# Optimization experiments

Measured on AMD Instinct MI355X. Metric: run time of the kernel, lower is better.

The kernel has to match this reference:

```python
import jax, jax.numpy as jnp
import numpy as np

N = 65536      # number of nodes being updated
EMBED = 1024   # embed_size
G = 256        # g_size (per-head dim)
MLP = 256      # mlp_size
H = 4          # n_head


def setup_inputs() -> dict:
    key = jax.random.key(0)
    ks = jax.random.split(key, 8)
    s_in = 1.0 / np.sqrt(EMBED)
    s_g = 1.0 / np.sqrt(G)
    s_m = 1.0 / np.sqrt(MLP)
    s_hg = 1.0 / np.sqrt(H * G)
    return {
        "q": jax.random.normal(ks[0], (N, EMBED), jnp.float32),
        "rep": jax.random.normal(ks[1], (N, EMBED), jnp.float32),
        "Wq": jax.random.normal(ks[2], (EMBED, H * G), jnp.float32) * s_in,
        "Wk": jax.random.normal(ks[3], (EMBED, H * G), jnp.float32) * s_in,
        "Wv": jax.random.normal(ks[4], (EMBED, H * G), jnp.float32) * s_in,
        "W1": jax.random.normal(ks[5], (H, G, MLP), jnp.float32) * s_g,
        "b1": jnp.zeros((H, MLP), jnp.float32),
        "W2": jax.random.normal(ks[6], (H, MLP, G), jnp.float32) * s_m,
        "b2": jnp.zeros((H, G), jnp.float32),
        "Ws": jax.random.normal(ks[7], (H * G, EMBED), jnp.float32) * s_hg,
    }


def reference(q, rep, Wq, Wk, Wv, W1, b1, W2, b2, Ws):
    # Per-head Q/K/V projections: [N, E] -> [N, H, G]
    n = q.shape[0]
    Qh = (q @ Wq).reshape(n, H, G)
    Kh = (rep @ Wk).reshape(n, H, G)
    Vh = (rep @ Wv).reshape(n, H, G)
    # Elementwise scaled attention gate (Q, K are per-node vectors -> 2D attn)
    gate = jax.nn.sigmoid(Qh * Kh * (1.0 / np.sqrt(G)))
    z = gate * Vh  # [N, H, G]
    # Per-head MLP (num_mlp = 1 block): G -> MLP -> G with ReLU
    h1 = jax.nn.relu(jnp.einsum('nhg,hgm->nhm', z, W1) + b1)
    z2 = jnp.einsum('nhm,hmg->nhg', h1, W2) + b2
    update_gate = z2.reshape(n, H * G)
    # update_attn_scale (no bias) + fused residual: h = Q - K + proj(gate)
    h = q - rep + update_gate @ Ws
    return h
```

## Files before the change

kernel.cpp:

```cpp
#include <hip/hip_runtime.h>
#include <hip/hip_bf16.h>


typedef __attribute__((ext_vector_type(8))) short bf16x8;
typedef __attribute__((ext_vector_type(4))) float f32x4;
typedef __attribute__((ext_vector_type(4))) short short4v;

static __device__ __forceinline__ short f2b(float x) {
  __hip_bfloat16 h = __float2bfloat16(x);
  return __builtin_bit_cast(short, h);
}
static __device__ __forceinline__ float b2f(short s) {
  unsigned u = ((unsigned)(unsigned short)s) << 16;
  return __builtin_bit_cast(float, u);
}

static __device__ __forceinline__ void stage_half(
    const short* __restrict__ g, long ld, short* dst, int wave, int lane)
{
  const int rw = lane >> 2;
  const int gg = (lane & 3) ^ ((rw >> 1) & 3);
  const short* gl = g + (long)rw * ld + (gg << 3);
  #pragma unroll
  for (int j = 0; j < 2; ++j) {
    const int r0 = j * 128 + wave * 16;
    __builtin_amdgcn_global_load_lds(
        (const __attribute__((address_space(1))) void*)(gl + (long)r0 * ld),
        (__attribute__((address_space(3))) void*)(dst + r0 * 32),
        16, 0, 0);
  }
}

static __device__ __forceinline__ void stage_half128(
    const short* __restrict__ g, long ld, short* dst, int wave, int lane)
{
  const int rw = lane >> 2;
  const int gg = (lane & 3) ^ ((rw >> 1) & 3);
  const int r0 = wave * 16;
  __builtin_amdgcn_global_load_lds(
      (const __attribute__((address_space(1))) void*)(g + (long)(r0 + rw) * ld + (gg << 3)),
      (__attribute__((address_space(3))) void*)(dst + r0 * 32),
      16, 0, 0);
}

__global__ void cvt_bf16(const float* __restrict__ in, short* __restrict__ out, long n) {
  long i = ((long)blockIdx.x * blockDim.x + threadIdx.x) * 4;
  const long stride = (long)gridDim.x * blockDim.x * 4;
  for (; i < n; i += stride) {
    float4 v = *(const float4*)(in + i);
    short4v o = { f2b(v.x), f2b(v.y), f2b(v.z), f2b(v.w) };
    *(short4v*)(out + i) = o;
  }
}

__global__ void prep_weights(
    const float* __restrict__ Wq, const float* __restrict__ Wk, const float* __restrict__ Wv,
    const float* __restrict__ W1, const float* __restrict__ W2, const float* __restrict__ Ws,
    short* __restrict__ wqt, short* __restrict__ wkt, short* __restrict__ wvt,
    short* __restrict__ w1t, short* __restrict__ w2t, short* __restrict__ wst)
{
  const int job = blockIdx.z;
  const float* src; short* dst; int R, C;
  if (job < 3)       { src = (job==0)?Wq:((job==1)?Wk:Wv); dst = (job==0)?wqt:((job==1)?wkt:wvt); R = 1024; C = 1024; }
  else if (job == 3) { src = Ws; dst = wst; R = 1024; C = 1024; }
  else if (job < 8)  { int h = job-4; src = W1 + h*65536; dst = w1t + h*65536; R = 256; C = 256; }
  else               { int h = job-8; src = W2 + h*65536; dst = w2t + h*65536; R = 256; C = 256; }
  const int c0 = blockIdx.x * 32, r0 = blockIdx.y * 32;
  if (c0 >= C || r0 >= R) return;
  __shared__ float t[32][33];
  for (int i = threadIdx.y; i < 32; i += 8)
    t[i][threadIdx.x] = src[(long)(r0 + i) * C + c0 + threadIdx.x];
  __syncthreads();
  for (int i = threadIdx.y; i < 32; i += 8)
    dst[(long)(c0 + i) * R + r0 + threadIdx.x] = f2b(t[threadIdx.x][i]);
}

template <int KDIM, bool RELU, bool BIAS, bool RESID, bool SWZ>
__global__ __launch_bounds__(512, 2) void gemm_bf16(
    const short* __restrict__ A, long lda, long zsa,
    const short* __restrict__ Bt, long ldb, long zsb,
    void* __restrict__ outv, long ldc, long zsc,
    const float* __restrict__ bias, long zsbias,
    const short* __restrict__ qres, const short* __restrict__ rres)
{
  __shared__ __align__(16) short lA[2][2][8192];
  __shared__ __align__(16) short lB[2][2][8192];
  const int lane = threadIdx.x & 63, wave = threadIdx.x >> 6;
  const int wm = wave >> 2, wn = wave & 3;
  int bx = blockIdx.x, by = blockIdx.y;
  if (SWZ) {
    const int nbx = gridDim.x;
    const int flat = by * nbx + bx;
    const int chunk = (int)(gridDim.x * gridDim.y) >> 3;
    const int fid = (flat & 7) * chunk + (flat >> 3);
    bx = fid % nbx; by = fid / nbx;
  }
  const long bm = (long)by * 256;
  const int  bn = bx * 256;
  const int  zi = blockIdx.z;

  const short* Ab = A + (long)zi * zsa + bm * lda;
  const short* Bb = Bt + (long)zi * zsb + (long)bn * ldb;
  constexpr int NT = KDIM / 64;
  const int g0 = lane >> 4;
  const int arow = wm * 128 + (lane & 15);
  const int bcol = wn * 64 + (lane & 15);

  auto stA = [&](int buf, int ks, int t) {
    const int tc = t < NT ? t : NT - 1;
    stage_half(Ab + tc * 64 + ks * 32, lda, &lA[buf][ks][0], wave, lane);
  };
  auto stB = [&](int buf, int ks, int t) {
    const int tc = t < NT ? t : NT - 1;
    stage_half(Bb + tc * 64 + ks * 32, ldb, &lB[buf][ks][0], wave, lane);
  };

  stA(0, 0, 0); stB(0, 0, 0); stA(0, 1, 0); stB(0, 1, 0);
  stA(1, 0, 1); stB(1, 0, 1);
  asm volatile("s_waitcnt vmcnt(4)" ::: "memory");
  __builtin_amdgcn_s_barrier();

  f32x4 acc[8][4] = {};
  bf16x8 b[4];

#define PHASE(BUF, MH, KS, LOADB, STAGE_STMT, CHECK)                        \
  {                                                                         \
    const short* aS = &lA[BUF][KS][0];                                      \
    const short* bS = &lB[BUF][KS][0];                                      \
    if (LOADB) {                                                            \
      _Pragma("unroll")                                                     \
      for (int j = 0; j < 4; ++j) {                                         \
        const int c = bcol + j * 16;                                        \
        b[j] = *(const bf16x8*)(bS + c * 32 + (((g0 ^ (c >> 1)) & 3) << 3));\
      }                                                                     \
    }                                                                       \
    bf16x8 a[4];                                                            \
    _Pragma("unroll")                                                       \
    for (int i2 = 0; i2 < 4; ++i2) {                                        \
      const int r = arow + (MH) * 64 + i2 * 16;                             \
      a[i2] = *(const bf16x8*)(aS + r * 32 + (((g0 ^ (r >> 1)) & 3) << 3)); \
    }                                                                       \
    STAGE_STMT;                                                             \
    if (CHECK) asm volatile("s_waitcnt vmcnt(4)" ::: "memory");             \
    asm volatile("" ::: "memory");                                          \
    __builtin_amdgcn_s_barrier();                                           \
    asm volatile("s_waitcnt lgkmcnt(0)" ::: "memory");                      \
    __builtin_amdgcn_sched_barrier(0);                                      \
    __builtin_amdgcn_s_setprio(1);                                          \
    _Pragma("unroll")                                                       \
    for (int i2 = 0; i2 < 4; ++i2)                                          \
      _Pragma("unroll")                                                     \
      for (int j = 0; j < 4; ++j)                                           \
        acc[(MH) * 4 + i2][j] = __builtin_amdgcn_mfma_f32_16x16x32_bf16(    \
            a[i2], b[j], acc[(MH) * 4 + i2][j], 0, 0, 0);                   \
    __builtin_amdgcn_s_setprio(0);                                          \
    asm volatile("" ::: "memory");                                          \
    __builtin_amdgcn_s_barrier();                                           \
  }

  for (int t = 0; t < NT; t += 2) {
    PHASE(0, 0, 0, true,  stA(1, 1, t + 1), false)
    PHASE(0, 1, 0, false, stB(1, 1, t + 1), false)
    PHASE(0, 0, 1, true,  stA(0, 0, t + 2), false)
    PHASE(0, 1, 1, false, stB(0, 0, t + 2), true)
    PHASE(1, 0, 0, true,  stA(0, 1, t + 2), false)
    PHASE(1, 1, 0, false, stB(0, 1, t + 2), false)
    PHASE(1, 0, 1, true,  stA(1, 0, t + 3), false)
    PHASE(1, 1, 1, false, stB(1, 0, t + 3), true)
  }
#undef PHASE

  #pragma unroll
  for (int i = 0; i < 8; ++i)
    #pragma unroll
    for (int j = 0; j < 4; ++j)
      #pragma unroll
      for (int r = 0; r < 4; ++r) {
        const int rl = wm * 128 + i * 16 + ((lane >> 4) << 2) + r;
        const int cl = wn * 64 + j * 16 + (lane & 15);
        float v = acc[i][j][r];
        if (BIAS) v += bias[(long)zi * zsbias + bn + cl];
        if (RELU) v = v > 0.0f ? v : 0.0f;
        const long row = bm + rl;
        const long gi = (long)zi * zsc + row * ldc + bn + cl;
        if (RESID) {
          ((float*)outv)[gi] = b2f(qres[gi]) - b2f(rres[gi]) + v;
        } else {
          ((short*)outv)[gi] = f2b(v);
        }
      }
}

__global__ __launch_bounds__(512, 2) void gemm_g23(
    const short* __restrict__ rb,
    const short* __restrict__ wkt,
    const short* __restrict__ wvt,
    const short* __restrict__ gh,
    short* __restrict__ zb)
{
  __shared__ __align__(16) short lA[2][2][8192];
  __shared__ __align__(16) short lK[2][2][4096];
  __shared__ __align__(16) short lV[2][2][4096];
  const int lane = threadIdx.x & 63, wave = threadIdx.x >> 6;
  const int wm = wave >> 2, wn = wave & 3;
  int bx = blockIdx.x, by = blockIdx.y;
  {
    const int flat = by * 8 + bx;
    const int chunk = (int)(gridDim.x * gridDim.y) >> 3;
    const int fid = (flat & 7) * chunk + (flat >> 3);
    bx = fid & 7; by = fid >> 3;
  }
  const long bm = (long)by * 256;
  const int  bn = bx * 128;

  const short* Ab = rb + bm * 1024;
  const short* Kb = wkt + (long)bn * 1024;
  const short* Vb = wvt + (long)bn * 1024;
  constexpr int NT = 16;
  const int g0 = lane >> 4;
  const int arow = wm * 128 + (lane & 15);
  const int bcol = wn * 32 + (lane & 15);

  auto stA = [&](int buf, int ks, int t) {
    const int tc = t < NT ? t : NT - 1;
    stage_half(Ab + tc * 64 + ks * 32, 1024, &lA[buf][ks][0], wave, lane);
  };
  auto stK = [&](int buf, int ks, int t) {
    const int tc = t < NT ? t : NT - 1;
    stage_half128(Kb + tc * 64 + ks * 32, 1024, &lK[buf][ks][0], wave, lane);
  };
  auto stV = [&](int buf, int ks, int t) {
    const int tc = t < NT ? t : NT - 1;
    stage_half128(Vb + tc * 64 + ks * 32, 1024, &lV[buf][ks][0], wave, lane);
  };

  stA(0, 0, 0); stK(0, 0, 0); stV(0, 0, 0);
  stA(0, 1, 0); stK(0, 1, 0); stV(0, 1, 0);
  stA(1, 0, 1); stK(1, 0, 1); stV(1, 0, 1);
  asm volatile("s_waitcnt vmcnt(4)" ::: "memory");
  __builtin_amdgcn_s_barrier();

  f32x4 ack[8][2] = {};
  f32x4 acv[8][2] = {};
  bf16x8 bk[2], bv[2];

#define PHASEG(BUF, MH, KS, LOADB, STAGE_STMT, CHECK)                       \
  {                                                                         \
    const short* aS = &lA[BUF][KS][0];                                      \
    if (LOADB) {                                                            \
      _Pragma("unroll")                                                     \
      for (int j = 0; j < 2; ++j) {                                         \
        const int c = bcol + j * 16;                                        \
        const int so = c * 32 + (((g0 ^ (c >> 1)) & 3) << 3);               \
        bk[j] = *(const bf16x8*)(&lK[BUF][KS][0] + so);                     \
        bv[j] = *(const bf16x8*)(&lV[BUF][KS][0] + so);                     \
      }                                                                     \
    }                                                                       \
    bf16x8 a[4];                                                            \
    _Pragma("unroll")                                                       \
    for (int i2 = 0; i2 < 4; ++i2) {                                        \
      const int r = arow + (MH) * 64 + i2 * 16;                             \
      a[i2] = *(const bf16x8*)(aS + r * 32 + (((g0 ^ (r >> 1)) & 3) << 3)); \
    }                                                                       \
    STAGE_STMT;                                                             \
    if (CHECK) asm volatile("s_waitcnt vmcnt(4)" ::: "memory");             \
    asm volatile("" ::: "memory");                                          \
    __builtin_amdgcn_s_barrier();                                           \
    asm volatile("s_waitcnt lgkmcnt(0)" ::: "memory");                      \
    __builtin_amdgcn_sched_barrier(0);                                      \
    __builtin_amdgcn_s_setprio(1);                                          \
    _Pragma("unroll")                                                       \
    for (int i2 = 0; i2 < 4; ++i2)                                          \
      _Pragma("unroll")                                                     \
      for (int j = 0; j < 2; ++j) {                                         \
        ack[(MH) * 4 + i2][j] = __builtin_amdgcn_mfma_f32_16x16x32_bf16(    \
            a[i2], bk[j], ack[(MH) * 4 + i2][j], 0, 0, 0);                  \
        acv[(MH) * 4 + i2][j] = __builtin_amdgcn_mfma_f32_16x16x32_bf16(    \
            a[i2], bv[j], acv[(MH) * 4 + i2][j], 0, 0, 0);                  \
      }                                                                     \
    __builtin_amdgcn_s_setprio(0);                                          \
    asm volatile("" ::: "memory");                                          \
    __builtin_amdgcn_s_barrier();                                           \
  }

  for (int t = 0; t < NT; t += 2) {
    PHASEG(0, 0, 0, true,  stA(1, 1, t + 1), false)
    PHASEG(0, 1, 0, false, { stK(1, 1, t + 1); stV(1, 1, t + 1); }, false)
    PHASEG(0, 0, 1, true,  stA(0, 0, t + 2), false)
    PHASEG(0, 1, 1, false, { stK(0, 0, t + 2); stV(0, 0, t + 2); }, true)
    PHASEG(1, 0, 0, true,  stA(0, 1, t + 2), false)
    PHASEG(1, 1, 0, false, { stK(0, 1, t + 2); stV(0, 1, t + 2); }, false)
    PHASEG(1, 0, 1, true,  stA(1, 0, t + 3), false)
    PHASEG(1, 1, 1, false, { stK(1, 0, t + 3); stV(1, 0, t + 3); }, true)
  }
#undef PHASEG

  #pragma unroll
  for (int i = 0; i < 8; ++i)
    #pragma unroll
    for (int j = 0; j < 2; ++j)
      #pragma unroll
      for (int r = 0; r < 4; ++r) {
        const int rl = wm * 128 + i * 16 + ((lane >> 4) << 2) + r;
        const int cl = wn * 32 + j * 16 + (lane & 15);
        const long gi = (bm + rl) * 1024 + bn + cl;
        const float x = b2f(gh[gi]) * ack[i][j][r] * 0.0625f;
        const float gate = 1.0f / (1.0f + __expf(-x));
        zb[gi] = f2b(gate * acv[i][j][r]);
      }
}

extern "C" void kernel_launch(void* const* d_in, const int* in_sizes, int n_in,
                              void* d_out, int out_size, void* d_ws, size_t ws_size,
                              hipStream_t stream) {
  const float* q   = (const float*)d_in[0];
  const float* rep = (const float*)d_in[1];
  const float* Wq  = (const float*)d_in[2];
  const float* Wk  = (const float*)d_in[3];
  const float* Wv  = (const float*)d_in[4];
  const float* W1  = (const float*)d_in[5];
  const float* b1  = (const float*)d_in[6];
  const float* W2  = (const float*)d_in[7];
  const float* b2  = (const float*)d_in[8];
  const float* Ws  = (const float*)d_in[9];
  float* out = (float*)d_out;

  const long NE = 67108864L;
  char* ws = (char*)d_ws;
  short* qb  = (short*)(ws);
  short* rb  = (short*)(ws + NE * 2);
  short* gh  = (short*)(ws + NE * 4);
  short* zb  = (short*)(ws + NE * 6);
  short* h1b = gh;
  short* ugb = zb;
  char*  wp  = ws + NE * 8;
  short* wqt = (short*)(wp);
  short* wkt = (short*)(wp + 2097152);
  short* wvt = (short*)(wp + 4194304);
  short* wst = (short*)(wp + 6291456);
  short* w1t = (short*)(wp + 8388608);
  short* w2t = (short*)(wp + 8912896);

  cvt_bf16<<<4096, 256, 0, stream>>>(q,   qb, NE);
  cvt_bf16<<<4096, 256, 0, stream>>>(rep, rb, NE);
  prep_weights<<<dim3(32, 32, 12), dim3(32, 8), 0, stream>>>(
      Wq, Wk, Wv, W1, W2, Ws, wqt, wkt, wvt, w1t, w2t, wst);

  gemm_bf16<1024, false, false, false, true><<<dim3(4, 256), 512, 0, stream>>>(
      qb, 1024, 0, wqt, 1024, 0, gh, 1024, 0, nullptr, 0, nullptr, nullptr);
  gemm_g23<<<dim3(8, 256), 512, 0, stream>>>(rb, wkt, wvt, gh, zb);

  gemm_bf16<256, true, true, false, false><<<dim3(1, 256, 4), 512, 0, stream>>>(
      zb, 1024, 256, w1t, 256, 65536, h1b, 1024, 256, b1, 256, nullptr, nullptr);
  gemm_bf16<256, false, true, false, false><<<dim3(1, 256, 4), 512, 0, stream>>>(
      h1b, 1024, 256, w2t, 256, 65536, ugb, 1024, 256, b2, 256, nullptr, nullptr);
  gemm_bf16<1024, false, false, true, true><<<dim3(4, 256), 512, 0, stream>>>(
      ugb, 1024, 0, wst, 1024, 0, out, 1024, 0, nullptr, 0, qb, rb);
}
```

Before: 1.044 ms.

## Restructure GEMM prefetch schedule to one barrier per phase with grouped staging

Both GEMM kernels (the generic one and the fused K/V gate kernel) now issue A and B staging for a whole k-slice together in one phase. Previously the loads were spread across phases. The prologue prefetches one fewer slice. Each phase now drops its trailing barrier and waits on lgkmcnt before the remaining barrier instead of after it. The aim is to halve the barrier count and simplify the double-buffer schedule, at the cost of a shallower prefetch lead and possible LDS write-after-read hazards now that the post-MFMA barrier is gone.

```diff
diff --git a/kernel.cpp b/kernel.cpp
--- a/kernel.cpp
+++ b/kernel.cpp
@@ -115,15 +115,15 @@
     stage_half(Bb + tc * 64 + ks * 32, ldb, &lB[buf][ks][0], wave, lane);
   };
 
-  stA(0, 0, 0); stB(0, 0, 0); stA(0, 1, 0); stB(0, 1, 0);
-  stA(1, 0, 1); stB(1, 0, 1);
+  stA(0, 0, 0); stB(0, 0, 0);
+  stA(0, 1, 0); stB(0, 1, 0);
   asm volatile("s_waitcnt vmcnt(4)" ::: "memory");
   __builtin_amdgcn_s_barrier();
 
   f32x4 acc[8][4] = {};
   bf16x8 b[4];
 
-#define PHASE(BUF, MH, KS, LOADB, STAGE_STMT, CHECK)                        \
+#define PHASE(BUF, MH, KS, LOADB, STAGE_STMT, DOVM)                         \
   {                                                                         \
     const short* aS = &lA[BUF][KS][0];                                      \
     const short* bS = &lB[BUF][KS][0];                                      \
@@ -141,10 +141,9 @@
       a[i2] = *(const bf16x8*)(aS + r * 32 + (((g0 ^ (r >> 1)) & 3) << 3)); \
     }                                                                       \
     STAGE_STMT;                                                             \
-    if (CHECK) asm volatile("s_waitcnt vmcnt(4)" ::: "memory");             \
-    asm volatile("" ::: "memory");                                          \
+    if (DOVM) asm volatile("s_waitcnt vmcnt(4)" ::: "memory");              \
+    asm volatile("s_waitcnt lgkmcnt(0)" ::: "memory");                      \
     __builtin_amdgcn_s_barrier();                                           \
-    asm volatile("s_waitcnt lgkmcnt(0)" ::: "memory");                      \
     __builtin_amdgcn_sched_barrier(0);                                      \
     __builtin_amdgcn_s_setprio(1);                                          \
     _Pragma("unroll")                                                       \
@@ -155,18 +154,17 @@
             a[i2], b[j], acc[(MH) * 4 + i2][j], 0, 0, 0);                   \
     __builtin_amdgcn_s_setprio(0);                                          \
     asm volatile("" ::: "memory");                                          \
-    __builtin_amdgcn_s_barrier();                                           \
   }
 
   for (int t = 0; t < NT; t += 2) {
-    PHASE(0, 0, 0, true,  stA(1, 1, t + 1), false)
-    PHASE(0, 1, 0, false, stB(1, 1, t + 1), false)
-    PHASE(0, 0, 1, true,  stA(0, 0, t + 2), false)
-    PHASE(0, 1, 1, false, stB(0, 0, t + 2), true)
-    PHASE(1, 0, 0, true,  stA(0, 1, t + 2), false)
-    PHASE(1, 1, 0, false, stB(0, 1, t + 2), false)
-    PHASE(1, 0, 1, true,  stA(1, 0, t + 3), false)
-    PHASE(1, 1, 1, false, stB(1, 0, t + 3), true)
+    PHASE(0, 0, 0, true,  { stA(1, 0, t + 1); stB(1, 0, t + 1); }, false)
+    PHASE(0, 1, 0, false, {}, true)
+    PHASE(0, 0, 1, true,  { stA(1, 1, t + 1); stB(1, 1, t + 1); }, false)
+    PHASE(0, 1, 1, false, {}, true)
+    PHASE(1, 0, 0, true,  { stA(0, 0, t + 2); stB(0, 0, t + 2); }, false)
+    PHASE(1, 1, 0, false, {}, true)
+    PHASE(1, 0, 1, true,  { stA(0, 1, t + 2); stB(0, 1, t + 2); }, false)
+    PHASE(1, 1, 1, false, {}, true)
   }
 #undef PHASE
 
@@ -221,22 +219,15 @@
   const int arow = wm * 128 + (lane & 15);
   const int bcol = wn * 32 + (lane & 15);
 
-  auto stA = [&](int buf, int ks, int t) {
+  auto stAll = [&](int buf, int ks, int t) {
     const int tc = t < NT ? t : NT - 1;
     stage_half(Ab + tc * 64 + ks * 32, 1024, &lA[buf][ks][0], wave, lane);
-  };
-  auto stK = [&](int buf, int ks, int t) {
-    const int tc = t < NT ? t : NT - 1;
     stage_half128(Kb + tc * 64 + ks * 32, 1024, &lK[buf][ks][0], wave, lane);
-  };
-  auto stV = [&](int buf, int ks, int t) {
-    const int tc = t < NT ? t : NT - 1;
     stage_half128(Vb + tc * 64 + ks * 32, 1024, &lV[buf][ks][0], wave, lane);
   };
 
-  stA(0, 0, 0); stK(0, 0, 0); stV(0, 0, 0);
-  stA(0, 1, 0); stK(0, 1, 0); stV(0, 1, 0);
-  stA(1, 0, 1); stK(1, 0, 1); stV(1, 0, 1);
+  stAll(0, 0, 0);
+  stAll(0, 1, 0);
   asm volatile("s_waitcnt vmcnt(4)" ::: "memory");
   __builtin_amdgcn_s_barrier();
 
@@ -244,7 +235,7 @@
   f32x4 acv[8][2] = {};
   bf16x8 bk[2], bv[2];
 
-#define PHASEG(BUF, MH, KS, LOADB, STAGE_STMT, CHECK)                       \
+#define PHASEG(BUF, MH, KS, LOADB, STAGE_STMT, DOVM)                        \
   {                                                                         \
     const short* aS = &lA[BUF][KS][0];                                      \
     if (LOADB) {                                                            \
@@ -263,10 +254,9 @@
       a[i2] = *(const bf16x8*)(aS + r * 32 + (((g0 ^ (r >> 1)) & 3) << 3)); \
     }                                                                       \
     STAGE_STMT;                                                             \
-    if (CHECK) asm volatile("s_waitcnt vmcnt(4)" ::: "memory");             \
-    asm volatile("" ::: "memory");                                          \
+    if (DOVM) asm volatile("s_waitcnt vmcnt(4)" ::: "memory");              \
+    asm volatile("s_waitcnt lgkmcnt(0)" ::: "memory");                      \
     __builtin_amdgcn_s_barrier();                                           \
-    asm volatile("s_waitcnt lgkmcnt(0)" ::: "memory");                      \
     __builtin_amdgcn_sched_barrier(0);                                      \
     __builtin_amdgcn_s_setprio(1);                                          \
     _Pragma("unroll")                                                       \
@@ -280,18 +270,17 @@
       }                                                                     \
     __builtin_amdgcn_s_setprio(0);                                          \
     asm volatile("" ::: "memory");                                          \
-    __builtin_amdgcn_s_barrier();                                           \
   }
 
   for (int t = 0; t < NT; t += 2) {
-    PHASEG(0, 0, 0, true,  stA(1, 1, t + 1), false)
-    PHASEG(0, 1, 0, false, { stK(1, 1, t + 1); stV(1, 1, t + 1); }, false)
-    PHASEG(0, 0, 1, true,  stA(0, 0, t + 2), false)
-    PHASEG(0, 1, 1, false, { stK(0, 0, t + 2); stV(0, 0, t + 2); }, true)
-    PHASEG(1, 0, 0, true,  stA(0, 1, t + 2), false)
-    PHASEG(1, 1, 0, false, { stK(0, 1, t + 2); stV(0, 1, t + 2); }, false)
-    PHASEG(1, 0, 1, true,  stA(1, 0, t + 3), false)
-    PHASEG(1, 1, 1, false, { stK(1, 0, t + 3); stV(1, 0, t + 3); }, true)
+    PHASEG(0, 0, 0, true,  stAll(1, 0, t + 1), false)
+    PHASEG(0, 1, 0, false, {}, true)
+    PHASEG(0, 0, 1, true,  stAll(1, 1, t + 1), false)
+    PHASEG(0, 1, 1, false, {}, true)
+    PHASEG(1, 0, 0, true,  stAll(0, 0, t + 2), false)
+    PHASEG(1, 1, 0, false, {}, true)
+    PHASEG(1, 0, 1, true,  stAll(0, 1, t + 2), false)
+    PHASEG(1, 1, 1, false, {}, true)
   }
 #undef PHASEG
 
```

New measurement: 1.109 ms. 6.3% more time.
